# Kernel optimization log

Hardware: AMD Instinct MI355X
Metric: run time of the kernel (lower is better)

Reference implementation:

```python
import jax, jax.numpy as jnp
import numpy as np

N = 8192

def setup_inputs() -> dict:
    key = jax.random.key(0)
    k1, k2, k3 = jax.random.split(key, 3)
    hazards = jax.random.normal(k1, (N, 1), dtype=jnp.float32)
    time = jax.random.uniform(k2, (N,), dtype=jnp.float32)
    c = jax.random.randint(k3, (N,), 0, 2, dtype=jnp.int32)
    return {"hazards": hazards, "time": time, "c": c}

def reference(hazards, time, c):
    # theta: [N] log-risk scores
    theta = hazards.reshape(-1)
    exp_theta = jnp.exp(theta)
    # Risk-set mask R[i, j] = (time[j] >= time[i]); built as one broadcasted
    # comparison instead of the original N^2 scalar writes.
    R = (time[None, :] >= time[:, None]).astype(theta.dtype)  # [N, N]
    # Row-wise masked exp-sum: sum_j exp(theta_j) * R[i, j]
    risk_sum = R @ exp_theta  # [N]
    loss_cox = -jnp.mean((theta - jnp.log(risk_sum)) * c.astype(theta.dtype))
    return loss_cox
```

## Files before the change

### kernel.cpp

```cpp
#include <hip/hip_runtime.h>
#include <math.h>

constexpr int CN = 8192;
constexpr int JC = 512;
constexpr int NJ = CN / JC;
constexpr int IB = 256;

__global__ __launch_bounds__(IB) void risk_kernel(
    const float* __restrict__ hazards,
    const float* __restrict__ time_,
    float* __restrict__ risk) {
  __shared__ float t_s[JC];
  __shared__ float e_s[JC];
  const int tid = threadIdx.x;
  const int jbase = blockIdx.y * JC;

  #pragma unroll
  for (int k = tid; k < JC; k += IB) {
    t_s[k] = time_[jbase + k];
    e_s[k] = expf(hazards[jbase + k]);
  }
  __syncthreads();

  const int i = blockIdx.x * IB + tid;
  const float ti = time_[i];

  float acc = 0.f;
  const float4* t4 = reinterpret_cast<const float4*>(t_s);
  const float4* e4 = reinterpret_cast<const float4*>(e_s);
  #pragma unroll 8
  for (int k = 0; k < JC / 4; ++k) {
    float4 t = t4[k];
    float4 e = e4[k];
    acc += (t.x >= ti) ? e.x : 0.f;
    acc += (t.y >= ti) ? e.y : 0.f;
    acc += (t.z >= ti) ? e.z : 0.f;
    acc += (t.w >= ti) ? e.w : 0.f;
  }
  atomicAdd(&risk[i], acc);
}

__global__ __launch_bounds__(1024) void loss_kernel(
    const float* __restrict__ hazards,
    const int* __restrict__ c,
    const float* __restrict__ risk,
    float* __restrict__ out) {
  const int tid = threadIdx.x;
  float partial = 0.f;
  for (int i = tid; i < CN; i += 1024) {
    if (c[i] != 0) partial += hazards[i] - logf(risk[i]);
  }
  #pragma unroll
  for (int off = 32; off > 0; off >>= 1)
    partial += __shfl_down(partial, off, 64);
  __shared__ float wsum[16];
  if ((tid & 63) == 0) wsum[tid >> 6] = partial;
  __syncthreads();
  if (tid == 0) {
    float s = 0.f;
    #pragma unroll
    for (int w = 0; w < 16; ++w) s += wsum[w];
    out[0] = -s / (float)CN;
  }
}

__global__ __launch_bounds__(256) void fused_kernel(
    const float* __restrict__ hazards,
    const float* __restrict__ time_,
    const int* __restrict__ c,
    float* __restrict__ out) {
  __shared__ float t_s[CN];
  __shared__ float e_s[CN];
  const int tid = threadIdx.x;
  for (int k = tid; k < CN; k += 256) {
    t_s[k] = time_[k];
    e_s[k] = expf(hazards[k]);
  }
  __syncthreads();

  const int i = blockIdx.x * 256 + tid;
  const float ti = time_[i];
  float acc = 0.f;
  const float4* t4 = reinterpret_cast<const float4*>(t_s);
  const float4* e4 = reinterpret_cast<const float4*>(e_s);
  #pragma unroll 8
  for (int k = 0; k < CN / 4; ++k) {
    float4 t = t4[k];
    float4 e = e4[k];
    acc += (t.x >= ti) ? e.x : 0.f;
    acc += (t.y >= ti) ? e.y : 0.f;
    acc += (t.z >= ti) ? e.z : 0.f;
    acc += (t.w >= ti) ? e.w : 0.f;
  }
  float contrib = (c[i] != 0) ? (hazards[i] - logf(acc)) : 0.f;
  #pragma unroll
  for (int off = 32; off > 0; off >>= 1)
    contrib += __shfl_down(contrib, off, 64);
  __shared__ float wsum[4];
  if ((tid & 63) == 0) wsum[tid >> 6] = contrib;
  __syncthreads();
  if (tid == 0) {
    float s = wsum[0] + wsum[1] + wsum[2] + wsum[3];
    atomicAdd(out, -s / (float)CN);
  }
}

extern "C" void kernel_launch(void* const* d_in, const int* in_sizes, int n_in,
                              void* d_out, int out_size, void* d_ws, size_t ws_size,
                              hipStream_t stream) {
  const float* hazards = (const float*)d_in[0];
  const float* time_   = (const float*)d_in[1];
  const int*   c       = (const int*)d_in[2];
  float* out = (float*)d_out;

  if (ws_size >= CN * sizeof(float)) {
    float* risk = (float*)d_ws;
    hipMemsetAsync(risk, 0, CN * sizeof(float), stream);
    risk_kernel<<<dim3(CN / IB, NJ), IB, 0, stream>>>(hazards, time_, risk);
    loss_kernel<<<1, 1024, 0, stream>>>(hazards, c, risk, out);
  } else {
    hipMemsetAsync(out, 0, sizeof(float), stream);
    fused_kernel<<<CN / 256, 256, 0, stream>>>(hazards, time_, c, out);
  }
}
```

Baseline: 71.57 us.

## Register-block four rows per thread and shrink j-chunks in risk kernel

Each thread now computes four output rows, so every float4 of time and exp values read from shared memory is reused across four comparisons. The j-chunk size drops from 512 to 128, which gives 64 chunks and 512 blocks in total. The intent is to cut LDS traffic per useful op and add independent accumulators for ILP. In exchange there are more blocks, each recomputing exp for its chunk, more atomics per output element, and higher register use. The loss kernel loop is also fully unrolled.

```diff
diff --git a/kernel.cpp b/kernel.cpp
--- a/kernel.cpp
+++ b/kernel.cpp
@@ -2,42 +2,62 @@
 #include <math.h>
 
 constexpr int CN = 8192;
-constexpr int JC = 512;
+constexpr int JC = 128;
 constexpr int NJ = CN / JC;
-constexpr int IB = 256;
+constexpr int TPB = 256;
+constexpr int IPT = 4;
+constexpr int ITILE = TPB * IPT;
+constexpr int NI = CN / ITILE;
 
-__global__ __launch_bounds__(IB) void risk_kernel(
+__global__ __launch_bounds__(TPB) void risk_kernel(
     const float* __restrict__ hazards,
     const float* __restrict__ time_,
     float* __restrict__ risk) {
-  __shared__ float t_s[JC];
-  __shared__ float e_s[JC];
+  __shared__ __align__(16) float t_s[JC];
+  __shared__ __align__(16) float e_s[JC];
   const int tid = threadIdx.x;
   const int jbase = blockIdx.y * JC;
 
-  #pragma unroll
-  for (int k = tid; k < JC; k += IB) {
-    t_s[k] = time_[jbase + k];
-    e_s[k] = expf(hazards[jbase + k]);
+  if (tid < JC) {
+    t_s[tid] = time_[jbase + tid];
+    e_s[tid] = expf(hazards[jbase + tid]);
   }
   __syncthreads();
 
-  const int i = blockIdx.x * IB + tid;
-  const float ti = time_[i];
+  const int ibase = blockIdx.x * ITILE + tid;
+  const float ti0 = time_[ibase];
+  const float ti1 = time_[ibase + 256];
+  const float ti2 = time_[ibase + 512];
+  const float ti3 = time_[ibase + 768];
 
-  float acc = 0.f;
+  float a0 = 0.f, a1 = 0.f, a2 = 0.f, a3 = 0.f;
   const float4* t4 = reinterpret_cast<const float4*>(t_s);
   const float4* e4 = reinterpret_cast<const float4*>(e_s);
-  #pragma unroll 8
+  #pragma unroll 4
   for (int k = 0; k < JC / 4; ++k) {
     float4 t = t4[k];
     float4 e = e4[k];
-    acc += (t.x >= ti) ? e.x : 0.f;
-    acc += (t.y >= ti) ? e.y : 0.f;
-    acc += (t.z >= ti) ? e.z : 0.f;
-    acc += (t.w >= ti) ? e.w : 0.f;
+    a0 += (t.x >= ti0) ? e.x : 0.f;
+    a0 += (t.y >= ti0) ? e.y : 0.f;
+    a0 += (t.z >= ti0) ? e.z : 0.f;
+    a0 += (t.w >= ti0) ? e.w : 0.f;
+    a1 += (t.x >= ti1) ? e.x : 0.f;
+    a1 += (t.y >= ti1) ? e.y : 0.f;
+    a1 += (t.z >= ti1) ? e.z : 0.f;
+    a1 += (t.w >= ti1) ? e.w : 0.f;
+    a2 += (t.x >= ti2) ? e.x : 0.f;
+    a2 += (t.y >= ti2) ? e.y : 0.f;
+    a2 += (t.z >= ti2) ? e.z : 0.f;
+    a2 += (t.w >= ti2) ? e.w : 0.f;
+    a3 += (t.x >= ti3) ? e.x : 0.f;
+    a3 += (t.y >= ti3) ? e.y : 0.f;
+    a3 += (t.z >= ti3) ? e.z : 0.f;
+    a3 += (t.w >= ti3) ? e.w : 0.f;
   }
-  atomicAdd(&risk[i], acc);
+  atomicAdd(&risk[ibase],       a0);
+  atomicAdd(&risk[ibase + 256], a1);
+  atomicAdd(&risk[ibase + 512], a2);
+  atomicAdd(&risk[ibase + 768], a3);
 }
 
 __global__ __launch_bounds__(1024) void loss_kernel(
@@ -47,7 +67,9 @@
     float* __restrict__ out) {
   const int tid = threadIdx.x;
   float partial = 0.f;
-  for (int i = tid; i < CN; i += 1024) {
+  #pragma unroll
+  for (int k = 0; k < CN / 1024; ++k) {
+    const int i = tid + k * 1024;
     if (c[i] != 0) partial += hazards[i] - logf(risk[i]);
   }
   #pragma unroll
@@ -69,8 +91,8 @@
     const float* __restrict__ time_,
     const int* __restrict__ c,
     float* __restrict__ out) {
-  __shared__ float t_s[CN];
-  __shared__ float e_s[CN];
+  __shared__ __align__(16) float t_s[CN];
+  __shared__ __align__(16) float e_s[CN];
   const int tid = threadIdx.x;
   for (int k = tid; k < CN; k += 256) {
     t_s[k] = time_[k];
@@ -116,7 +138,7 @@
   if (ws_size >= CN * sizeof(float)) {
     float* risk = (float*)d_ws;
     hipMemsetAsync(risk, 0, CN * sizeof(float), stream);
-    risk_kernel<<<dim3(CN / IB, NJ), IB, 0, stream>>>(hazards, time_, risk);
+    risk_kernel<<<dim3(NI, NJ), TPB, 0, stream>>>(hazards, time_, risk);
     loss_kernel<<<1, 1024, 0, stream>>>(hazards, c, risk, out);
   } else {
     hipMemsetAsync(out, 0, sizeof(float), stream);
```

Result: faster. 70.15 us (-2.0%).
